# Performance work log

Measured on AMD Instinct MI355X. Metric: run time of the kernel, lower is better.

The kernel has to match this reference:

```python
import jax, jax.numpy as jnp
import numpy as np

VOCAB = 100000
HID = 128
BATCH = 1024


def setup_inputs() -> dict:
    key = jax.random.key(0)
    ks = jax.random.split(key, 8)
    s = 1.0 / np.sqrt(HID)  # torch nn.GRU / nn.Linear uniform init scale
    inp = {
        "input": jax.random.randint(ks[0], (BATCH,), 0, VOCAB),
        "hidden": jax.random.normal(ks[1], (1, BATCH, HID), dtype=jnp.float32),
        # GRU params (PyTorch layout: gates ordered r, z, n along first axis)
        "W_ih": jax.random.uniform(ks[2], (3 * HID, VOCAB), jnp.float32, -s, s),
        "b_ih": jax.random.uniform(ks[3], (3 * HID,), jnp.float32, -s, s),
        "W_hh": jax.random.uniform(ks[4], (3 * HID, HID), jnp.float32, -s, s),
        "b_hh": jax.random.uniform(ks[5], (3 * HID,), jnp.float32, -s, s),
        # hidden2output Linear
        "W_out": jax.random.uniform(ks[6], (VOCAB, HID), jnp.float32, -s, s),
        "b_out": jax.random.uniform(ks[7], (VOCAB,), jnp.float32, -s, s),
    }
    return inp


def reference(input, hidden, W_ih, b_ih, W_hh, b_hh, W_out, b_out):
    # encode(): one-hot of `input` over the vocab. A one-hot @ W_ih.T is
    # mathematically a row-gather of W_ih.T, so we gather instead of
    # materializing the (B, VOCAB) one-hot and doing a dense matmul.
    gi = W_ih.T[input] + b_ih            # (B, 3H)  == onehot @ W_ih.T + b_ih
    h0 = hidden[0]                       # (B, H), single layer, seq_len=1
    gh = h0 @ W_hh.T + b_hh              # (B, 3H)
    i_r, i_z, i_n = jnp.split(gi, 3, axis=-1)
    h_r, h_z, h_n = jnp.split(gh, 3, axis=-1)
    r = jax.nn.sigmoid(i_r + h_r)
    z = jax.nn.sigmoid(i_z + h_z)
    n = jnp.tanh(i_n + r * h_n)
    h_new = (1.0 - z) * n + z * h0       # (B, H)
    # output.view(-1, H) -> logits = ReLU(Linear(h_new))
    logit = jax.nn.relu(h_new @ W_out.T + b_out)  # (B, VOCAB)
    return logit, h_new[None]            # hidden: (layers=1, B, H)
```

## Files before the change

kernel.cpp:

```cpp
#include <hip/hip_runtime.h>
#include <hip/hip_bf16.h>
#include <stdint.h>

#define VOCAB 100000
#define HID 128
#define BATCH 1024

typedef __attribute__((ext_vector_type(8))) short short8;
typedef __attribute__((ext_vector_type(4))) float float4v;
typedef __attribute__((ext_vector_type(16))) float float16v;

__device__ __forceinline__ unsigned short f2bf_rne(float f) {
    union { float f; uint32_t u; } v; v.f = f;
    uint32_t u = v.u;
    u += 0x7fffu + ((u >> 16) & 1u);
    return (unsigned short)(u >> 16);
}

__global__ __launch_bounds__(256) void gru_kernel(
    const int* __restrict__ idx,
    const float* __restrict__ h0,
    const float* __restrict__ W_ih,
    const float* __restrict__ b_ih,
    const float* __restrict__ W_hh,
    const float* __restrict__ b_hh,
    float* __restrict__ h_out,
    unsigned short* __restrict__ h_bf)
{
    const int t  = threadIdx.x;
    const int u  = t >> 1;
    const int kh = t & 1;
    const int b0 = blockIdx.x * 4;

    __shared__ float hs[4][HID];
    for (int r = t >> 7; r < 4; r += 2)
        hs[r][t & 127] = h0[(size_t)(b0 + r) * HID + (t & 127)];

    float gi[2][3];
    #pragma unroll
    for (int i = 0; i < 2; ++i) {
        int b  = b0 + kh * 2 + i;
        int ix = idx[b];
        #pragma unroll
        for (int g = 0; g < 3; ++g)
            gi[i][g] = W_ih[(size_t)(g * HID + u) * VOCAB + ix] + b_ih[g * HID + u];
    }

    __syncthreads();

    float acc[4][3];
    #pragma unroll
    for (int r = 0; r < 4; ++r)
        #pragma unroll
        for (int g = 0; g < 3; ++g)
            acc[r][g] = 0.f;

    const int kbase = kh * 64;
    #pragma unroll 4
    for (int i = 0; i < 16; ++i) {
        int k = kbase + i * 4;
        float4v w[3];
        #pragma unroll
        for (int g = 0; g < 3; ++g)
            w[g] = *(const float4v*)&W_hh[(size_t)(g * HID + u) * HID + k];
        #pragma unroll
        for (int r = 0; r < 4; ++r) {
            float4v h = *(const float4v*)&hs[r][k];
            #pragma unroll
            for (int g = 0; g < 3; ++g)
                acc[r][g] += w[g][0]*h[0] + w[g][1]*h[1] + w[g][2]*h[2] + w[g][3]*h[3];
        }
    }

    #pragma unroll
    for (int r = 0; r < 4; ++r)
        #pragma unroll
        for (int g = 0; g < 3; ++g)
            acc[r][g] += __shfl_xor(acc[r][g], 1, 64);

    const float bh_r = b_hh[u];
    const float bh_z = b_hh[HID + u];
    const float bh_n = b_hh[2 * HID + u];

    #pragma unroll
    for (int i = 0; i < 2; ++i) {
        int r = kh * 2 + i;
        float gh_r = acc[r][0] + bh_r;
        float gh_z = acc[r][1] + bh_z;
        float gh_n = acc[r][2] + bh_n;
        float rr = 1.f / (1.f + expf(-(gi[i][0] + gh_r)));
        float zz = 1.f / (1.f + expf(-(gi[i][1] + gh_z)));
        float nn = tanhf(gi[i][2] + rr * gh_n);
        float hp = hs[r][u];
        float hn = (1.f - zz) * nn + zz * hp;
        size_t o = (size_t)(b0 + r) * HID + u;
        h_out[o] = hn;
        h_bf[o]  = f2bf_rne(hn);
    }
}

__global__ __launch_bounds__(256) void out_gemm_kernel(
    const unsigned short* __restrict__ A,
    const float* __restrict__ W,
    const float* __restrict__ bias,
    float* __restrict__ out)
{
    const int lane = threadIdx.x & 63;
    const int wave = threadIdx.x >> 6;
    const int m0   = blockIdx.x * 64;
    const int n0   = blockIdx.y * 128 + wave * 32;

    const int l31 = lane & 31;
    const int lhi = lane >> 5;

    const int v  = n0 + l31;
    const int vc = v < VOCAB ? v : (VOCAB - 1);

    float16v acc0, acc1;
    #pragma unroll
    for (int i = 0; i < 16; ++i) { acc0[i] = 0.f; acc1[i] = 0.f; }

    const unsigned short* Ap0 = A + (size_t)(m0 + l31) * HID + lhi * 8;
    const unsigned short* Ap1 = Ap0 + 32 * HID;
    const float*          Wp  = W + (size_t)vc * HID + lhi * 8;

    #pragma unroll
    for (int kk = 0; kk < 8; ++kk) {
        const int k = kk * 16;
        short8 a0 = *(const short8*)(Ap0 + k);
        short8 a1 = *(const short8*)(Ap1 + k);
        float4v w0 = *(const float4v*)(Wp + k);
        float4v w1 = *(const float4v*)(Wp + k + 4);
        short8 b;
        #pragma unroll
        for (int j = 0; j < 4; ++j) {
            b[j]     = (short)f2bf_rne(w0[j]);
            b[j + 4] = (short)f2bf_rne(w1[j]);
        }
        acc0 = __builtin_amdgcn_mfma_f32_32x32x16_bf16(a0, b, acc0, 0, 0, 0);
        acc1 = __builtin_amdgcn_mfma_f32_32x32x16_bf16(a1, b, acc1, 0, 0, 0);
    }

    if (v < VOCAB) {
        const float bv = bias[vc];
        float* outb = out + (size_t)m0 * VOCAB + v;
        #pragma unroll
        for (int r = 0; r < 16; ++r) {
            int mrow = (r & 3) + 8 * (r >> 2) + 4 * lhi;
            float v0 = acc0[r] + bv; v0 = v0 > 0.f ? v0 : 0.f;
            float v1 = acc1[r] + bv; v1 = v1 > 0.f ? v1 : 0.f;
            outb[(size_t)mrow * VOCAB]        = v0;
            outb[(size_t)(mrow + 32) * VOCAB] = v1;
        }
    }
}

extern "C" void kernel_launch(void* const* d_in, const int* in_sizes, int n_in,
                              void* d_out, int out_size, void* d_ws, size_t ws_size,
                              hipStream_t stream) {
    const int*   idx   = (const int*)d_in[0];
    const float* h0    = (const float*)d_in[1];
    const float* W_ih  = (const float*)d_in[2];
    const float* b_ih  = (const float*)d_in[3];
    const float* W_hh  = (const float*)d_in[4];
    const float* b_hh  = (const float*)d_in[5];
    const float* W_out = (const float*)d_in[6];
    const float* b_out = (const float*)d_in[7];

    float* out = (float*)d_out;
    unsigned short* hbf = (unsigned short*)d_ws;

    gru_kernel<<<BATCH / 4, 256, 0, stream>>>(
        idx, h0, W_ih, b_ih, W_hh, b_hh,
        out + (size_t)BATCH * VOCAB, hbf);

    dim3 grid(BATCH / 64, (VOCAB + 127) / 128);
    out_gemm_kernel<<<grid, 256, 0, stream>>>(hbf, W_out, b_out, out);
}
```

Before: 683.8 us.

## Pre-convert W_out to bf16 in prep kernel and use nontemporal output stores

```diff
diff --git a/kernel.cpp b/kernel.cpp
--- a/kernel.cpp
+++ b/kernel.cpp
@@ -5,6 +5,10 @@
 #define VOCAB 100000
 #define HID 128
 #define BATCH 1024
+
+#define W_ELTS (VOCAB * HID)
+#define CONV_BLOCKS (W_ELTS / 2048)
+#define GRU_BLOCKS (BATCH / 4)
 
 typedef __attribute__((ext_vector_type(8))) short short8;
 typedef __attribute__((ext_vector_type(4))) float float4v;
@@ -17,17 +21,34 @@
     return (unsigned short)(u >> 16);
 }
 
-__global__ __launch_bounds__(256) void gru_kernel(
+__global__ __launch_bounds__(256) void prep_kernel(
     const int* __restrict__ idx,
     const float* __restrict__ h0,
     const float* __restrict__ W_ih,
     const float* __restrict__ b_ih,
     const float* __restrict__ W_hh,
     const float* __restrict__ b_hh,
+    const float* __restrict__ W_out,
     float* __restrict__ h_out,
+    unsigned short* __restrict__ W_bf,
     unsigned short* __restrict__ h_bf)
 {
-    const int t  = threadIdx.x;
+    const int t = threadIdx.x;
+
+    if (blockIdx.x >= GRU_BLOCKS) {
+        const size_t base = ((size_t)(blockIdx.x - GRU_BLOCKS) * 256 + t) * 8;
+        float4v w0 = *(const float4v*)(W_out + base);
+        float4v w1 = *(const float4v*)(W_out + base + 4);
+        short8 b;
+        #pragma unroll
+        for (int j = 0; j < 4; ++j) {
+            b[j]     = (short)f2bf_rne(w0[j]);
+            b[j + 4] = (short)f2bf_rne(w1[j]);
+        }
+        *(short8*)(W_bf + base) = b;
+        return;
+    }
+
     const int u  = t >> 1;
     const int kh = t & 1;
     const int b0 = blockIdx.x * 4;
@@ -101,7 +122,7 @@
 
 __global__ __launch_bounds__(256) void out_gemm_kernel(
     const unsigned short* __restrict__ A,
-    const float* __restrict__ W,
+    const unsigned short* __restrict__ Wb,
     const float* __restrict__ bias,
     float* __restrict__ out)
 {
@@ -122,21 +143,14 @@
 
     const unsigned short* Ap0 = A + (size_t)(m0 + l31) * HID + lhi * 8;
     const unsigned short* Ap1 = Ap0 + 32 * HID;
-    const float*          Wp  = W + (size_t)vc * HID + lhi * 8;
+    const unsigned short* Wp  = Wb + (size_t)vc * HID + lhi * 8;
 
     #pragma unroll
     for (int kk = 0; kk < 8; ++kk) {
         const int k = kk * 16;
         short8 a0 = *(const short8*)(Ap0 + k);
         short8 a1 = *(const short8*)(Ap1 + k);
-        float4v w0 = *(const float4v*)(Wp + k);
-        float4v w1 = *(const float4v*)(Wp + k + 4);
-        short8 b;
-        #pragma unroll
-        for (int j = 0; j < 4; ++j) {
-            b[j]     = (short)f2bf_rne(w0[j]);
-            b[j + 4] = (short)f2bf_rne(w1[j]);
-        }
+        short8 b  = *(const short8*)(Wp + k);
         acc0 = __builtin_amdgcn_mfma_f32_32x32x16_bf16(a0, b, acc0, 0, 0, 0);
         acc1 = __builtin_amdgcn_mfma_f32_32x32x16_bf16(a1, b, acc1, 0, 0, 0);
     }
@@ -149,8 +163,8 @@
             int mrow = (r & 3) + 8 * (r >> 2) + 4 * lhi;
             float v0 = acc0[r] + bv; v0 = v0 > 0.f ? v0 : 0.f;
             float v1 = acc1[r] + bv; v1 = v1 > 0.f ? v1 : 0.f;
-            outb[(size_t)mrow * VOCAB]        = v0;
-            outb[(size_t)(mrow + 32) * VOCAB] = v1;
+            __builtin_nontemporal_store(v0, outb + (size_t)mrow * VOCAB);
+            __builtin_nontemporal_store(v1, outb + (size_t)(mrow + 32) * VOCAB);
         }
     }
 }
@@ -168,12 +182,13 @@
     const float* b_out = (const float*)d_in[7];
 
     float* out = (float*)d_out;
-    unsigned short* hbf = (unsigned short*)d_ws;
+    unsigned short* W_bf = (unsigned short*)d_ws;
+    unsigned short* h_bf = (unsigned short*)d_ws + W_ELTS;
 
-    gru_kernel<<<BATCH / 4, 256, 0, stream>>>(
-        idx, h0, W_ih, b_ih, W_hh, b_hh,
-        out + (size_t)BATCH * VOCAB, hbf);
+    prep_kernel<<<GRU_BLOCKS + CONV_BLOCKS, 256, 0, stream>>>(
+        idx, h0, W_ih, b_ih, W_hh, b_hh, W_out,
+        out + (size_t)BATCH * VOCAB, W_bf, h_bf);
 
     dim3 grid(BATCH / 64, (VOCAB + 127) / 128);
-    out_gemm_kernel<<<grid, 256, 0, stream>>>(hbf, W_out, b_out, out);
+    out_gemm_kernel<<<grid, 256, 0, stream>>>(h_bf, W_bf, b_out, out);
 }
```

Result: faster. 624.5 us (-8.7%).
